# Kernel optimization log

Measured on AMD Instinct MI355X. Metric: run time of the kernel, lower is better.

The kernel has to match this reference:

```python
import jax, jax.numpy as jnp
import numpy as np

EPS = 1e-12
SHRINK = 0.0025

def _l2norm(x, axis=1):
    return x / jnp.maximum(jnp.linalg.norm(x, axis=axis, keepdims=True), EPS)

def setup_inputs() -> dict:
    key = jax.random.key(0)
    ks = jax.random.split(key, 6)
    N, C, H, W = 32, 512, 32, 32
    mem_dim, spatial = 512, H * W
    hid = spatial // 2
    x = jax.random.normal(ks[0], (N, C, H, W), dtype=jnp.float32)
    memory = jax.random.normal(ks[1], (mem_dim, spatial), dtype=jnp.float32)
    memory = _l2norm(memory, axis=1)  # buffer is L2-normalized at init
    w1 = jax.random.normal(ks[2], (hid, spatial), dtype=jnp.float32) * 0.02
    b1 = jax.random.normal(ks[3], (hid,), dtype=jnp.float32) * 0.02
    w2 = jax.random.normal(ks[4], (spatial, hid), dtype=jnp.float32) * 0.02
    b2 = jax.random.normal(ks[5], (spatial,), dtype=jnp.float32) * 0.02
    return {"x": x, "memory": memory, "w1": w1, "b1": b1, "w2": w2, "b2": b2}

def reference(x, memory, w1, b1, w2, b2):
    N, C, H, W = x.shape
    mem_dim = memory.shape[0]
    input_flat = x.reshape(N * C, H * W)
    input_norm = _l2norm(input_flat, axis=1)
    # shared MLP over memory bank: Linear -> ReLU -> Linear -> ReLU
    h = jax.nn.relu(memory @ w1.T + b1)
    mem_proc = jax.nn.relu(h @ w2.T + b2)
    memory_norm = _l2norm(mem_proc, axis=1)
    # addressing: cosine sim -> softmax -> hard shrink -> L1 renorm
    att = jax.nn.softmax(input_norm @ memory_norm.T, axis=1)  # [N*C, M]
    att = jax.nn.relu(att - SHRINK)
    att = att / jnp.maximum(att.sum(axis=1, keepdims=True), EPS)  # p=1 norm (att >= 0)
    output = (att @ memory_norm).reshape(N, C, H, W)
    att_channel_avg = att.reshape(N, C, mem_dim).mean(axis=1)  # [N, M]
    att_spatial = jnp.broadcast_to(att_channel_avg[:, :, None, None], (N, mem_dim, H, W))
    return output, att_spatial, input_flat, memory_norm, att
```

## Files before the change

### kernel.cpp

```cpp
#include <hip/hip_runtime.h>

typedef float  f32x4  __attribute__((ext_vector_type(4)));
typedef __bf16 bf16x8 __attribute__((ext_vector_type(8)));
typedef __bf16 bf16x4 __attribute__((ext_vector_type(4)));

#define L2EPS   1e-12f
#define SHRINKC 0.0025f


__device__ __forceinline__ bf16x8 pack_bf16(f32x4 v0, f32x4 v1) {
  bf16x8 r;
  r[0] = (__bf16)v0[0]; r[1] = (__bf16)v0[1]; r[2] = (__bf16)v0[2]; r[3] = (__bf16)v0[3];
  r[4] = (__bf16)v1[0]; r[5] = (__bf16)v1[1]; r[6] = (__bf16)v1[2]; r[7] = (__bf16)v1[3];
  return r;
}

__device__ __forceinline__ bf16x8 load_cvt_bf16x8(const float* p) {
  const f32x4* q = (const f32x4*)p;
  return pack_bf16(q[0], q[1]);
}

__device__ __forceinline__ float dot4(f32x4 v) {
  return v[0]*v[0] + v[1]*v[1] + v[2]*v[2] + v[3]*v[3];
}

__global__ __launch_bounds__(64) void gemm1(
    const float* __restrict__ A, const float* __restrict__ B,
    const float* __restrict__ bias, float* __restrict__ C,
    float* __restrict__ attsum) {
  const int bid = blockIdx.y * gridDim.x + blockIdx.x;
  attsum[bid * 64 + threadIdx.x] = 0.f;

  const int K = 1024, N = 512;
  const int r0   = blockIdx.x * 32;
  const int n0   = blockIdx.y * 32;
  const int lane = threadIdx.x & 63;
  const int quad = lane >> 4;
  const int m    = lane & 15;

  f32x4 acc[2][2] = {};
  for (int k0 = 0; k0 < K; k0 += 32) {
    const int kk = k0 + quad * 8;
    bf16x8 a[2], b[2];
    #pragma unroll
    for (int rg = 0; rg < 2; ++rg)
      a[rg] = load_cvt_bf16x8(A + (size_t)(r0 + rg * 16 + m) * K + kk);
    #pragma unroll
    for (int cf = 0; cf < 2; ++cf)
      b[cf] = load_cvt_bf16x8(B + (size_t)(n0 + cf * 16 + m) * K + kk);
    #pragma unroll
    for (int rg = 0; rg < 2; ++rg)
      #pragma unroll
      for (int cf = 0; cf < 2; ++cf)
        acc[rg][cf] = __builtin_amdgcn_mfma_f32_16x16x32_bf16(a[rg], b[cf], acc[rg][cf], 0, 0, 0);
  }
  #pragma unroll
  for (int rg = 0; rg < 2; ++rg)
    #pragma unroll
    for (int cf = 0; cf < 2; ++cf) {
      const int n = n0 + cf * 16 + m;
      const float bv = bias[n];
      #pragma unroll
      for (int vi = 0; vi < 4; ++vi) {
        const int r = r0 + rg * 16 + quad * 4 + vi;
        C[(size_t)r * N + n] = fmaxf(acc[rg][cf][vi] + bv, 0.f);
      }
    }
}

__global__ __launch_bounds__(64) void gemm2(
    const float* __restrict__ A, const float* __restrict__ B,
    const float* __restrict__ bias, float* __restrict__ C) {
  const int K = 512, N = 1024;
  const int r0   = blockIdx.x * 32;
  const int n0   = blockIdx.y * 32;
  const int lane = threadIdx.x & 63;
  const int quad = lane >> 4;
  const int m    = lane & 15;

  f32x4 acc[2][2] = {};
  for (int k0 = 0; k0 < K; k0 += 32) {
    const int kk = k0 + quad * 8;
    bf16x8 a[2], b[2];
    #pragma unroll
    for (int rg = 0; rg < 2; ++rg)
      a[rg] = load_cvt_bf16x8(A + (size_t)(r0 + rg * 16 + m) * K + kk);
    #pragma unroll
    for (int cf = 0; cf < 2; ++cf)
      b[cf] = load_cvt_bf16x8(B + (size_t)(n0 + cf * 16 + m) * K + kk);
    #pragma unroll
    for (int rg = 0; rg < 2; ++rg)
      #pragma unroll
      for (int cf = 0; cf < 2; ++cf)
        acc[rg][cf] = __builtin_amdgcn_mfma_f32_16x16x32_bf16(a[rg], b[cf], acc[rg][cf], 0, 0, 0);
  }
  #pragma unroll
  for (int rg = 0; rg < 2; ++rg)
    #pragma unroll
    for (int cf = 0; cf < 2; ++cf) {
      const int n = n0 + cf * 16 + m;
      const float bv = bias[n];
      #pragma unroll
      for (int vi = 0; vi < 4; ++vi) {
        const int r = r0 + rg * 16 + quad * 4 + vi;
        C[(size_t)r * N + n] = fmaxf(acc[rg][cf][vi] + bv, 0.f);
      }
    }
}

__global__ __launch_bounds__(256) void norm_rows(
    const float* __restrict__ mp, float* __restrict__ mn_f32,
    __bf16* __restrict__ mn_bf16) {
  const int r = blockIdx.x;
  const int tid = threadIdx.x;
  const f32x4 v = *(const f32x4*)(mp + (size_t)r * 1024 + tid * 4);
  float ss = dot4(v);
  #pragma unroll
  for (int d = 1; d < 64; d <<= 1) ss += __shfl_xor(ss, d);
  __shared__ float wsum[4];
  __shared__ float invs;
  if ((tid & 63) == 0) wsum[tid >> 6] = ss;
  __syncthreads();
  if (tid == 0) {
    float t = wsum[0] + wsum[1] + wsum[2] + wsum[3];
    invs = 1.f / fmaxf(sqrtf(t), L2EPS);
  }
  __syncthreads();
  const float iv = invs;
  f32x4 o = v * iv;
  *(f32x4*)(mn_f32 + (size_t)r * 1024 + tid * 4) = o;
  bf16x4 ob;
  ob[0] = (__bf16)o[0]; ob[1] = (__bf16)o[1]; ob[2] = (__bf16)o[2]; ob[3] = (__bf16)o[3];
  *(bf16x4*)(mn_bf16 + (size_t)r * 1024 + tid * 4) = ob;
}

__global__ __launch_bounds__(256) void attend(
    const float* __restrict__ x, const __bf16* __restrict__ Mn,
    const float* __restrict__ Mnf, float* __restrict__ out_flat,
    float* __restrict__ out_out, float* __restrict__ out_att,
    float* __restrict__ attsum) {
  __shared__ float red[2][4][32];
  const int r0   = blockIdx.x * 32;
  const int tid  = threadIdx.x;
  const int wave = tid >> 6;
  const int lane = tid & 63;
  const int quad = lane >> 4;
  const int m    = lane & 15;
  const int n0w  = wave * 128;

  float ss0 = 0.f, ss1 = 0.f;
  f32x4 acc[8][2] = {};
  for (int k0 = 0; k0 < 1024; k0 += 32) {
    const int kk = k0 + quad * 8;
    bf16x8 b[2];
    f32x4 v0a, v0b, v1a, v1b;
    {
      const f32x4* q = (const f32x4*)(x + (size_t)(r0 + m) * 1024 + kk);
      v0a = q[0]; v0b = q[1];
      b[0] = pack_bf16(v0a, v0b);
      ss0 += dot4(v0a) + dot4(v0b);
    }
    {
      const f32x4* q = (const f32x4*)(x + (size_t)(r0 + 16 + m) * 1024 + kk);
      v1a = q[0]; v1b = q[1];
      b[1] = pack_bf16(v1a, v1b);
      ss1 += dot4(v1a) + dot4(v1b);
    }
    if ((k0 >> 8) == wave) {
      float* d0 = out_flat + (size_t)(r0 + m) * 1024 + kk;
      float* d1 = out_flat + (size_t)(r0 + 16 + m) * 1024 + kk;
      __builtin_nontemporal_store(v0a, (f32x4*)d0);
      __builtin_nontemporal_store(v0b, (f32x4*)(d0 + 4));
      __builtin_nontemporal_store(v1a, (f32x4*)d1);
      __builtin_nontemporal_store(v1b, (f32x4*)(d1 + 4));
    }
    #pragma unroll
    for (int nf = 0; nf < 8; ++nf) {
      const bf16x8 a = *(const bf16x8*)(Mn + (size_t)(n0w + nf * 16 + m) * 1024 + kk);
      acc[nf][0] = __builtin_amdgcn_mfma_f32_16x16x32_bf16(a, b[0], acc[nf][0], 0, 0, 0);
      acc[nf][1] = __builtin_amdgcn_mfma_f32_16x16x32_bf16(a, b[1], acc[nf][1], 0, 0, 0);
    }
  }
  ss0 += __shfl_xor(ss0, 16); ss0 += __shfl_xor(ss0, 32);
  ss1 += __shfl_xor(ss1, 16); ss1 += __shfl_xor(ss1, 32);
  const float iv0 = 1.f / fmaxf(sqrtf(ss0), L2EPS);
  const float iv1 = 1.f / fmaxf(sqrtf(ss1), L2EPS);

  float se0 = 0.f, se1 = 0.f;
  #pragma unroll
  for (int nf = 0; nf < 8; ++nf)
    #pragma unroll
    for (int vi = 0; vi < 4; ++vi) {
      const float e0 = __expf(acc[nf][0][vi] * iv0);
      const float e1 = __expf(acc[nf][1][vi] * iv1);
      acc[nf][0][vi] = e0; acc[nf][1][vi] = e1;
      se0 += e0; se1 += e1;
    }
  se0 += __shfl_xor(se0, 16); se0 += __shfl_xor(se0, 32);
  se1 += __shfl_xor(se1, 16); se1 += __shfl_xor(se1, 32);
  if (quad == 0) { red[0][wave][m] = se0; red[0][wave][16 + m] = se1; }
  __syncthreads();
  const float te0 = red[0][0][m] + red[0][1][m] + red[0][2][m] + red[0][3][m];
  const float te1 = red[0][0][16 + m] + red[0][1][16 + m] + red[0][2][16 + m] + red[0][3][16 + m];
  const float ie0 = 1.f / te0;
  const float ie1 = 1.f / te1;

  float rs0 = 0.f, rs1 = 0.f;
  #pragma unroll
  for (int nf = 0; nf < 8; ++nf)
    #pragma unroll
    for (int vi = 0; vi < 4; ++vi) {
      const float s0 = fmaxf(acc[nf][0][vi] * ie0 - SHRINKC, 0.f);
      const float s1 = fmaxf(acc[nf][1][vi] * ie1 - SHRINKC, 0.f);
      acc[nf][0][vi] = s0; acc[nf][1][vi] = s1;
      rs0 += s0; rs1 += s1;
    }
  rs0 += __shfl_xor(rs0, 16); rs0 += __shfl_xor(rs0, 32);
  rs1 += __shfl_xor(rs1, 16); rs1 += __shfl_xor(rs1, 32);
  if (quad == 0) { red[1][wave][m] = rs0; red[1][wave][16 + m] = rs1; }
  __syncthreads();
  const float tr0 = red[1][0][m] + red[1][1][m] + red[1][2][m] + red[1][3][m];
  const float tr1 = red[1][0][16 + m] + red[1][1][16 + m] + red[1][2][16 + m] + red[1][3][16 + m];
  const float ir0 = 1.f / fmaxf(tr0, L2EPS);
  const float ir1 = 1.f / fmaxf(tr1, L2EPS);

  #pragma unroll
  for (int nf = 0; nf < 8; ++nf) {
    acc[nf][0] *= ir0;
    acc[nf][1] *= ir1;
    __builtin_nontemporal_store(acc[nf][0],
        (f32x4*)(out_att + (size_t)(r0 + m)      * 512 + n0w + nf * 16 + quad * 4));
    __builtin_nontemporal_store(acc[nf][1],
        (f32x4*)(out_att + (size_t)(r0 + 16 + m) * 512 + n0w + nf * 16 + quad * 4));
  }
  __threadfence_block();
  const int any = __syncthreads_or(tr0 + tr1 > 0.f);

  if (!any) {
    const f32x4 z = {0.f, 0.f, 0.f, 0.f};
    float* dst = out_out + (size_t)r0 * 1024;
    for (int idx = tid; idx < 32 * 1024 / 4; idx += 256)
      __builtin_nontemporal_store(z, (f32x4*)(dst + idx * 4));
  } else {
    const int nimg = r0 >> 9;
    #pragma unroll
    for (int nf = 0; nf < 8; ++nf) {
      f32x4 v = acc[nf][0] + acc[nf][1];
      #pragma unroll
      for (int d = 1; d < 16; d <<= 1) {
        v[0] += __shfl_xor(v[0], d); v[1] += __shfl_xor(v[1], d);
        v[2] += __shfl_xor(v[2], d); v[3] += __shfl_xor(v[3], d);
      }
      if (m == 0) {
        const int c = n0w + nf * 16 + quad * 4;
        atomicAdd(&attsum[nimg * 512 + c + 0], v[0]);
        atomicAdd(&attsum[nimg * 512 + c + 1], v[1]);
        atomicAdd(&attsum[nimg * 512 + c + 2], v[2]);
        atomicAdd(&attsum[nimg * 512 + c + 3], v[3]);
      }
    }
    const int c0 = tid * 4;
    for (int rr = 0; rr < 32; ++rr) {
      const float* arow = out_att + (size_t)(r0 + rr) * 512;
      f32x4 o = {0.f, 0.f, 0.f, 0.f};
      for (int mm = 0; mm < 512; ++mm) {
        const float a = arow[mm];
        o += a * (*(const f32x4*)(Mnf + (size_t)mm * 1024 + c0));
      }
      *(f32x4*)(out_out + (size_t)(r0 + rr) * 1024 + c0) = o;
    }
  }
}

__global__ __launch_bounds__(256) void spread(
    const float* __restrict__ attsum, float* __restrict__ out_sp) {
  const int base = blockIdx.x * 8;
  #pragma unroll
  for (int p = 0; p < 8; ++p) {
    const int nm = base + p;
    const float v = attsum[nm] * (1.f / 512.f);
    const f32x4 vv = {v, v, v, v};
    __builtin_nontemporal_store(vv, (f32x4*)(out_sp + (size_t)nm * 1024 + threadIdx.x * 4));
  }
}


extern "C" void kernel_launch(void* const* d_in, const int* in_sizes, int n_in,
                              void* d_out, int out_size, void* d_ws, size_t ws_size,
                              hipStream_t stream) {
  const float* x      = (const float*)d_in[0];
  const float* memory = (const float*)d_in[1];
  const float* w1     = (const float*)d_in[2];
  const float* b1     = (const float*)d_in[3];
  const float* w2     = (const float*)d_in[4];
  const float* b2     = (const float*)d_in[5];

  float* out = (float*)d_out;
  float* out_output = out;
  float* out_attsp  = out + 16777216;
  float* out_flat   = out + 33554432;
  float* out_mnorm  = out + 50331648;
  float* out_att    = out + 50855936;

  char* ws = (char*)d_ws;
  float*  h      = (float*)ws;
  float*  mp     = (float*)(ws + (1 << 20));
  __bf16* mnb    = (__bf16*)(ws + (1 << 20) + (2 << 20));
  float*  attsum = (float*)(ws + (1 << 20) + (2 << 20) + (1 << 20));

  gemm1<<<dim3(16, 16), 64, 0, stream>>>(memory, w1, b1, h, attsum);
  gemm2<<<dim3(16, 32), 64, 0, stream>>>(h, w2, b2, mp);
  norm_rows<<<512, 256, 0, stream>>>(mp, out_mnorm, mnb);
  attend<<<512, 256, 0, stream>>>(x, mnb, out_mnorm, out_flat, out_output, out_att, attsum);
  spread<<<2048, 256, 0, stream>>>(attsum, out_attsp);
}
```

Before: 404.3 us.

## Split input copy into separate kernel and prefetch x in attend loop

```diff
diff --git a/kernel.cpp b/kernel.cpp
--- a/kernel.cpp
+++ b/kernel.cpp
@@ -22,6 +22,17 @@
 
 __device__ __forceinline__ float dot4(f32x4 v) {
   return v[0]*v[0] + v[1]*v[1] + v[2]*v[2] + v[3]*v[3];
+}
+
+__global__ __launch_bounds__(256) void copy_flat(
+    const float* __restrict__ x, float* __restrict__ out_flat) {
+  const int stride = 2048 * 256;
+  int idx = blockIdx.x * 256 + threadIdx.x;
+  #pragma unroll
+  for (int i = 0; i < 8; ++i, idx += stride) {
+    const f32x4 v = *(const f32x4*)(x + (size_t)idx * 4);
+    __builtin_nontemporal_store(v, (f32x4*)(out_flat + (size_t)idx * 4));
+  }
 }
 
 __global__ __launch_bounds__(64) void gemm1(
@@ -136,9 +147,8 @@
 
 __global__ __launch_bounds__(256) void attend(
     const float* __restrict__ x, const __bf16* __restrict__ Mn,
-    const float* __restrict__ Mnf, float* __restrict__ out_flat,
-    float* __restrict__ out_out, float* __restrict__ out_att,
-    float* __restrict__ attsum) {
+    const float* __restrict__ Mnf, float* __restrict__ out_out,
+    float* __restrict__ out_att, float* __restrict__ attsum) {
   __shared__ float red[2][4][32];
   const int r0   = blockIdx.x * 32;
   const int tid  = threadIdx.x;
@@ -148,38 +158,39 @@
   const int m    = lane & 15;
   const int n0w  = wave * 128;
 
+  const float* xr0 = x + (size_t)(r0 + m) * 1024;
+  const float* xr1 = x + (size_t)(r0 + 16 + m) * 1024;
+
   float ss0 = 0.f, ss1 = 0.f;
   f32x4 acc[8][2] = {};
+  f32x4 c0a, c0b, c1a, c1b;
+  {
+    const int kk = quad * 8;
+    const f32x4* q0 = (const f32x4*)(xr0 + kk);
+    const f32x4* q1 = (const f32x4*)(xr1 + kk);
+    c0a = q0[0]; c0b = q0[1];
+    c1a = q1[0]; c1b = q1[1];
+  }
   for (int k0 = 0; k0 < 1024; k0 += 32) {
     const int kk = k0 + quad * 8;
-    bf16x8 b[2];
-    f32x4 v0a, v0b, v1a, v1b;
-    {
-      const f32x4* q = (const f32x4*)(x + (size_t)(r0 + m) * 1024 + kk);
-      v0a = q[0]; v0b = q[1];
-      b[0] = pack_bf16(v0a, v0b);
-      ss0 += dot4(v0a) + dot4(v0b);
-    }
-    {
-      const f32x4* q = (const f32x4*)(x + (size_t)(r0 + 16 + m) * 1024 + kk);
-      v1a = q[0]; v1b = q[1];
-      b[1] = pack_bf16(v1a, v1b);
-      ss1 += dot4(v1a) + dot4(v1b);
-    }
-    if ((k0 >> 8) == wave) {
-      float* d0 = out_flat + (size_t)(r0 + m) * 1024 + kk;
-      float* d1 = out_flat + (size_t)(r0 + 16 + m) * 1024 + kk;
-      __builtin_nontemporal_store(v0a, (f32x4*)d0);
-      __builtin_nontemporal_store(v0b, (f32x4*)(d0 + 4));
-      __builtin_nontemporal_store(v1a, (f32x4*)d1);
-      __builtin_nontemporal_store(v1b, (f32x4*)(d1 + 4));
-    }
+    f32x4 n0a, n0b, n1a, n1b;
+    if (k0 + 32 < 1024) {
+      const f32x4* q0 = (const f32x4*)(xr0 + kk + 32);
+      const f32x4* q1 = (const f32x4*)(xr1 + kk + 32);
+      n0a = q0[0]; n0b = q0[1];
+      n1a = q1[0]; n1b = q1[1];
+    }
+    bf16x8 b0 = pack_bf16(c0a, c0b);
+    bf16x8 b1 = pack_bf16(c1a, c1b);
+    ss0 += dot4(c0a) + dot4(c0b);
+    ss1 += dot4(c1a) + dot4(c1b);
     #pragma unroll
     for (int nf = 0; nf < 8; ++nf) {
       const bf16x8 a = *(const bf16x8*)(Mn + (size_t)(n0w + nf * 16 + m) * 1024 + kk);
-      acc[nf][0] = __builtin_amdgcn_mfma_f32_16x16x32_bf16(a, b[0], acc[nf][0], 0, 0, 0);
-      acc[nf][1] = __builtin_amdgcn_mfma_f32_16x16x32_bf16(a, b[1], acc[nf][1], 0, 0, 0);
-    }
+      acc[nf][0] = __builtin_amdgcn_mfma_f32_16x16x32_bf16(a, b0, acc[nf][0], 0, 0, 0);
+      acc[nf][1] = __builtin_amdgcn_mfma_f32_16x16x32_bf16(a, b1, acc[nf][1], 0, 0, 0);
+    }
+    c0a = n0a; c0b = n0b; c1a = n1a; c1b = n1b;
   }
   ss0 += __shfl_xor(ss0, 16); ss0 += __shfl_xor(ss0, 32);
   ss1 += __shfl_xor(ss1, 16); ss1 += __shfl_xor(ss1, 32);
@@ -308,9 +319,10 @@
   __bf16* mnb    = (__bf16*)(ws + (1 << 20) + (2 << 20));
   float*  attsum = (float*)(ws + (1 << 20) + (2 << 20) + (1 << 20));
 
+  copy_flat<<<2048, 256, 0, stream>>>(x, out_flat);
   gemm1<<<dim3(16, 16), 64, 0, stream>>>(memory, w1, b1, h, attsum);
   gemm2<<<dim3(16, 32), 64, 0, stream>>>(h, w2, b2, mp);
   norm_rows<<<512, 256, 0, stream>>>(mp, out_mnorm, mnb);
-  attend<<<512, 256, 0, stream>>>(x, mnb, out_mnorm, out_flat, out_output, out_att, attsum);
+  attend<<<512, 256, 0, stream>>>(x, mnb, out_mnorm, out_output, out_att, attsum);
   spread<<<2048, 256, 0, stream>>>(attsum, out_attsp);
 }
```

After: 424.3 us. 5.0% more time.
